# Performance work log

Measured on AMD Instinct MI355X. Metric: run time of the kernel, lower is better.

## Reference

```python
import jax, jax.numpy as jnp
import numpy as np

B, S, D, H = 4, 2048, 1024, 16
HD = D // H

def setup_inputs() -> dict:
    key = jax.random.key(0)
    ks = jax.random.split(key, 6)
    scale = 0.02
    return {
        "x": jax.random.normal(ks[0], (B, S, D), jnp.float32),
        "Wq": jax.random.normal(ks[1], (D, D), jnp.float32) * scale,
        "Wk": jax.random.normal(ks[2], (D, D), jnp.float32) * scale,
        "Wv": jax.random.normal(ks[3], (D, D), jnp.float32) * scale,
        "Wo": jax.random.normal(ks[4], (D, D), jnp.float32) * scale,
        "bo": jnp.zeros((D,), jnp.float32),
    }

def reference(x, Wq, Wk, Wv, Wo, bo):
    b, s, _ = x.shape
    # separate Q/K/V projections (no bias, qkv_bias=False)
    q = jnp.einsum('bsd,ed->bse', x, Wq).reshape(b, s, H, HD).transpose(0, 2, 1, 3)
    k = jnp.einsum('bsd,ed->bse', x, Wk).reshape(b, s, H, HD).transpose(0, 2, 1, 3)
    v = jnp.einsum('bsd,ed->bse', x, Wv).reshape(b, s, H, HD).transpose(0, 2, 1, 3)
    # full [B,H,S,S] scores, causal mask, scaled softmax (matches torch order:
    # mask applied to raw scores, then divide by sqrt(head_dim))
    scores = jnp.einsum('bhqd,bhkd->bhqk', q, k)
    causal = jnp.tril(jnp.ones((s, s), bool))
    scores = jnp.where(causal, scores, -jnp.inf)
    attn = jax.nn.softmax(scores / np.float32(np.sqrt(HD)), axis=-1)
    # dropout=0.0 -> identity in eval
    ctx = jnp.einsum('bhqk,bhkd->bhqd', attn, v)
    ctx = ctx.transpose(0, 2, 1, 3).reshape(b, s, D)
    return jnp.einsum('bsd,ed->bse', ctx, Wo) + bo
```

## Files before the change

### kernel.cpp

```cpp
#include <hip/hip_runtime.h>
#include <stdint.h>

#define DEVI __device__ __forceinline__

typedef __attribute__((ext_vector_type(8))) short bf16x8;
typedef __attribute__((ext_vector_type(8))) unsigned short u16x8;
typedef __attribute__((ext_vector_type(4))) float f32x4;
typedef unsigned short u16;
typedef unsigned int u32;

constexpr int B = 4, S = 2048, D = 1024, H = 16;
constexpr int BS = B * S;
constexpr int QS = 3 * D;
constexpr float CS = 0.18033688011112042f;

DEVI u16 f2bf(float f) {
  u32 u = __float_as_uint(f);
  u32 r = (u + 0x7FFFu + ((u >> 16) & 1u)) >> 16;
  return (u16)r;
}

DEVI void async_load16(const void* g, void* l) {
  __builtin_amdgcn_global_load_lds((const __attribute__((address_space(1))) u32*)g,
                                   (__attribute__((address_space(3))) u32*)l, 16, 0, 0);
}

__global__ void cast_f32_bf16(const float* __restrict__ in, u16* __restrict__ out, int n4) {
  int i = blockIdx.x * blockDim.x + threadIdx.x;
  if (i >= n4) return;
  float4 v = ((const float4*)in)[i];
  ushort4 o;
  o.x = f2bf(v.x); o.y = f2bf(v.y); o.z = f2bf(v.z); o.w = f2bf(v.w);
  ((ushort4*)out)[i] = o;
}

__global__ void cast_w4(const float* __restrict__ wq, const float* __restrict__ wk,
                        const float* __restrict__ wv, const float* __restrict__ wo,
                        u16* __restrict__ wqkv, u16* __restrict__ wob, int n4) {
  int i = blockIdx.x * blockDim.x + threadIdx.x;
  if (i >= n4) return;
  int y = blockIdx.y;
  const float* src = (y == 0) ? wq : (y == 1) ? wk : (y == 2) ? wv : wo;
  u16* dst = (y < 3) ? (wqkv + (size_t)y * D * D) : wob;
  float4 v = ((const float4*)src)[i];
  ushort4 o;
  o.x = f2bf(v.x); o.y = f2bf(v.y); o.z = f2bf(v.z); o.w = f2bf(v.w);
  ((ushort4*)dst)[i] = o;
}

template<int STORE_BF16, int ADD_BIAS, int SCALE_QCOLS>
__global__ __launch_bounds__(256)
void gemm_bt(const u16* __restrict__ A, const u16* __restrict__ Bt,
             const float* __restrict__ bias, void* __restrict__ Cout,
             int M, int N, int K) {
  __shared__ u16 a_lds[2][128 * 32];
  __shared__ u16 b_lds[2][128 * 32];
  const int tid = threadIdx.x, lane = tid & 63, wv = tid >> 6;
  const int m0 = blockIdx.x * 128, n0 = blockIdx.y * 128;
  const int wm = (wv >> 1) * 64, wn = (wv & 1) * 64;
  const int fr = lane & 15, fk = (lane >> 4) * 8;

  f32x4 acc[4][4] = {};

  const int seg = wv * 2;
  const int srow = seg * 16 + (lane >> 2);
  const int scolb = (lane & 3) * 16;
  const char* ab = (const char*)A + ((size_t)(m0 + srow) * K) * 2 + scolb;
  const char* bb = (const char*)Bt + ((size_t)(n0 + srow) * K) * 2 + scolb;
  const size_t row16 = (size_t)16 * K * 2;

  {
    char* adst = (char*)a_lds[0] + seg * 1024;
    char* bdst = (char*)b_lds[0] + seg * 1024;
    async_load16(ab, adst);
    async_load16(ab + row16, adst + 1024);
    async_load16(bb, bdst);
    async_load16(bb + row16, bdst + 1024);
    ab += 64; bb += 64;
  }
  int cur = 0;

  for (int k0 = 0; k0 < K; k0 += 32) {
    asm volatile("s_waitcnt vmcnt(0)" ::: "memory");
    asm volatile("s_barrier" ::: "memory");
    bf16x8 af[4], bfr[4];
    #pragma unroll
    for (int i = 0; i < 4; ++i) {
      af[i]  = *(const bf16x8*)&a_lds[cur][(wm + i * 16 + fr) * 32 + fk];
      bfr[i] = *(const bf16x8*)&b_lds[cur][(wn + i * 16 + fr) * 32 + fk];
    }
    if (k0 + 32 < K) {
      char* adst = (char*)a_lds[cur ^ 1] + seg * 1024;
      char* bdst = (char*)b_lds[cur ^ 1] + seg * 1024;
      async_load16(ab, adst);
      async_load16(ab + row16, adst + 1024);
      async_load16(bb, bdst);
      async_load16(bb + row16, bdst + 1024);
      ab += 64; bb += 64;
    }
    #pragma unroll
    for (int i = 0; i < 4; ++i)
      #pragma unroll
      for (int j = 0; j < 4; ++j)
        acc[i][j] = __builtin_amdgcn_mfma_f32_16x16x32_bf16(af[i], bfr[j], acc[i][j], 0, 0, 0);
    cur ^= 1;
  }

  const int cr = (lane >> 4) * 4, cc = lane & 15;
  const float qsc = (SCALE_QCOLS && n0 < 1024) ? CS : 1.0f;
  #pragma unroll
  for (int j = 0; j < 4; ++j) {
    int gn = n0 + wn + j * 16 + cc;
    float bv = ADD_BIAS ? bias[gn] : 0.0f;
    #pragma unroll
    for (int i = 0; i < 4; ++i) {
      #pragma unroll
      for (int r = 0; r < 4; ++r) {
        size_t idx = (size_t)(m0 + wm + i * 16 + cr + r) * N + gn;
        float v = acc[i][j][r];
        if (SCALE_QCOLS) v *= qsc;
        v += bv;
        if (STORE_BF16) ((u16*)Cout)[idx] = f2bf(v);
        else            ((float*)Cout)[idx] = v;
      }
    }
  }
}

__global__ __launch_bounds__(256, 2)
void attn_kernel(const u16* __restrict__ Q, const u16* __restrict__ K,
                 const u16* __restrict__ V, u16* __restrict__ C) {
  __shared__ u16 vt_lds[2][64 * 72];
  __shared__ u16 p_lds[4][32 * 72];

  const int tid = threadIdx.x, lane = tid & 63, wv = tid >> 6;
  const int f = blockIdx.x;
  const int pair = (f >> 3) & 7;
  const int g = (f & 7) | ((f >> 6) << 3);
  const int h = g & 15, b = g >> 4;

  const int fr = lane & 15, hi = lane >> 4, fk = hi * 8;
  const int cr = hi * 4, cc = fr;

  const size_t base = (size_t)(b * S) * QS + h * 64;
  const size_t cbase = (size_t)(b * S) * D + h * 64;

  const int vd0 = (tid & 7) * 8;
  const int vkvp = tid >> 3;
  const u16* Vg = V + base;
  const u16* Kg = K + base;

  for (int half = 0; half < 2; ++half) {
    const int qt = half ? (15 - pair) : pair;
    const int q0 = qt * 128;
    const int qw = q0 + wv * 32;

    bf16x8 qf[2][2];
    {
      const u16* Qp = Q + base + (size_t)qw * QS;
      #pragma unroll
      for (int mi = 0; mi < 2; ++mi)
        #pragma unroll
        for (int kc = 0; kc < 2; ++kc)
          qf[mi][kc] = *(const bf16x8*)(Qp + (size_t)(mi * 16 + fr) * QS + kc * 32 + fk);
    }

    f32x4 ctx[2][4] = {};
    float lr[2][4] = {};

    const int nt = q0 / 64 + 2;

    u16x8 v0a, v0b, v1a, v1b;
    {
      const u16* vr = Vg + (size_t)(vkvp * 2) * QS + vd0;
      v0a = *(const u16x8*)vr;
      v0b = *(const u16x8*)(vr + QS);
    }
    int cur = 0;

    for (int t = 0; t < nt; ++t) {
      const int kv0 = t * 64;
      const bool part = (kv0 <= qw + 31);
      const bool more = (t + 1 < nt);

      {
        #pragma unroll
        for (int i = 0; i < 8; ++i) {
          int d = vd0 + i;
          int kvp = vkvp ^ (((d >> 3) & 7) << 2);
          u32 w = (u32)(u16)v0a[i] | ((u32)(u16)v0b[i] << 16);
          *(u32*)&vt_lds[cur][d * 72 + kvp * 2] = w;
        }
      }

      bf16x8 kf[4][2];
      if (part) {
        const u16* kp = Kg + (size_t)(kv0 + fr) * QS + fk;
        #pragma unroll
        for (int ni = 0; ni < 4; ++ni)
          #pragma unroll
          for (int kc = 0; kc < 2; ++kc)
            kf[ni][kc] = *(const bf16x8*)(kp + (size_t)(ni * 16) * QS + kc * 32);
      }
      if (more) {
        const u16* vr = Vg + (size_t)((t + 1) * 64 + vkvp * 2) * QS + vd0;
        v1a = *(const u16x8*)vr;
        v1b = *(const u16x8*)(vr + QS);
      }

      asm volatile("s_waitcnt lgkmcnt(0)" ::: "memory");
      asm volatile("s_barrier" ::: "memory");

      if (part) {
        f32x4 sc[2][4] = {};
        __builtin_amdgcn_s_setprio(1);
        #pragma unroll
        for (int mi = 0; mi < 2; ++mi)
          #pragma unroll
          for (int ni = 0; ni < 4; ++ni)
            #pragma unroll
            for (int kc = 0; kc < 2; ++kc)
              sc[mi][ni] = __builtin_amdgcn_mfma_f32_16x16x32_bf16(qf[mi][kc], kf[ni][kc], sc[mi][ni], 0, 0, 0);
        __builtin_amdgcn_s_setprio(0);

        if (kv0 + 63 > qw) {
          #pragma unroll
          for (int mi = 0; mi < 2; ++mi)
            #pragma unroll
            for (int ni = 0; ni < 4; ++ni)
              #pragma unroll
              for (int r = 0; r < 4; ++r) {
                int qrow = qw + mi * 16 + cr + r;
                int kvc = kv0 + ni * 16 + cc;
                if (kvc > qrow) sc[mi][ni][r] = -3.0e38f;
              }
        }

        #pragma unroll
        for (int mi = 0; mi < 2; ++mi)
          #pragma unroll
          for (int ni = 0; ni < 4; ++ni)
            #pragma unroll
            for (int r = 0; r < 4; ++r)
              sc[mi][ni][r] = exp2f(sc[mi][ni][r]);
        #pragma unroll
        for (int mi = 0; mi < 2; ++mi)
          #pragma unroll
          for (int r = 0; r < 4; ++r) {
            float rs = (sc[mi][0][r] + sc[mi][1][r]) + (sc[mi][2][r] + sc[mi][3][r]);
            rs += __shfl_xor(rs, 1);
            rs += __shfl_xor(rs, 2);
            rs += __shfl_xor(rs, 4);
            rs += __shfl_xor(rs, 8);
            lr[mi][r] += rs;
          }

        #pragma unroll
        for (int mi = 0; mi < 2; ++mi)
          #pragma unroll
          for (int ni = 0; ni < 4; ++ni)
            #pragma unroll
            for (int r = 0; r < 4; ++r)
              p_lds[wv][(mi * 16 + cr + r) * 72 + ni * 16 + cc] = f2bf(sc[mi][ni][r]);

        asm volatile("s_waitcnt lgkmcnt(0)" ::: "memory");
        __builtin_amdgcn_sched_barrier(0);

        bf16x8 pa[2][2], vf[4][2];
        #pragma unroll
        for (int mi = 0; mi < 2; ++mi)
          #pragma unroll
          for (int kc = 0; kc < 2; ++kc)
            pa[mi][kc] = *(const bf16x8*)&p_lds[wv][(mi * 16 + fr) * 72 + kc * 32 + fk];
        #pragma unroll
        for (int db = 0; db < 4; ++db)
          #pragma unroll
          for (int kc = 0; kc < 2; ++kc) {
            int d = db * 16 + fr;
            int kvp = (kc * 16 + hi * 4) ^ (((d >> 3) & 7) << 2);
            vf[db][kc] = *(const bf16x8*)&vt_lds[cur][d * 72 + kvp * 2];
          }
        __builtin_amdgcn_s_setprio(1);
        #pragma unroll
        for (int mi = 0; mi < 2; ++mi)
          #pragma unroll
          for (int db = 0; db < 4; ++db)
            #pragma unroll
            for (int kc = 0; kc < 2; ++kc)
              ctx[mi][db] = __builtin_amdgcn_mfma_f32_16x16x32_bf16(pa[mi][kc], vf[db][kc], ctx[mi][db], 0, 0, 0);
        __builtin_amdgcn_s_setprio(0);
      }

      if (more) { v0a = v1a; v0b = v1b; }
      cur ^= 1;
    }

    u16* Cp = C + cbase + (size_t)qw * D;
    #pragma unroll
    for (int mi = 0; mi < 2; ++mi)
      #pragma unroll
      for (int r = 0; r < 4; ++r) {
        float inv = 1.0f / lr[mi][r];
        #pragma unroll
        for (int db = 0; db < 4; ++db)
          Cp[(size_t)(mi * 16 + cr + r) * D + db * 16 + cc] = f2bf(ctx[mi][db][r] * inv);
      }
  }
}

extern "C" void kernel_launch(void* const* d_in, const int* in_sizes, int n_in,
                              void* d_out, int out_size, void* d_ws, size_t ws_size,
                              hipStream_t stream) {
  const float* x  = (const float*)d_in[0];
  const float* Wq = (const float*)d_in[1];
  const float* Wk = (const float*)d_in[2];
  const float* Wv = (const float*)d_in[3];
  const float* Wo = (const float*)d_in[4];
  const float* bo = (const float*)d_in[5];

  char* ws = (char*)d_ws;
  u16* xb    = (u16*)(ws + 0);
  u16* Wqkvb = (u16*)(ws + (16u << 20));
  u16* Wob   = (u16*)(ws + (22u << 20));
  u16* QKVb  = (u16*)(ws + (24u << 20));
  u16* Cb    = (u16*)(ws + (72u << 20));

  const int XN = BS * D;
  const int WN = D * D;

  cast_f32_bf16<<<XN / 4 / 256, 256, 0, stream>>>(x, xb, XN / 4);
  cast_w4<<<dim3(WN / 4 / 256, 4), 256, 0, stream>>>(Wq, Wk, Wv, Wo, Wqkvb, Wob, WN / 4);

  gemm_bt<1, 0, 1><<<dim3(BS / 128, QS / 128), dim3(256), 0, stream>>>(xb, Wqkvb, nullptr, QKVb, BS, QS, D);

  attn_kernel<<<dim3(512), dim3(256), 0, stream>>>(QKVb, QKVb + D, QKVb + 2 * D, Cb);

  gemm_bt<0, 1, 0><<<dim3(BS / 128, D / 128), dim3(256), 0, stream>>>(Cb, Wob, bo, d_out, BS, D, D);
}
```

Before: 288.0 us.

## Shrink attention query tiles to 64 rows and triple-buffer GEMM LDS

The attention kernel now processes 64-row query tiles, with 16 rows per wave instead of 32. This doubles the grid to 1024 blocks and raises launch bounds to 4 blocks per CU, giving more parallelism and finer causal load balance at the cost of less K/V reuse per block. The GEMM moves from double- to triple-buffered LDS staging with a partial vmcnt wait, keeping two tiles of async loads in flight to hide global latency. This uses more LDS per block, which may reduce GEMM occupancy.

```diff
diff --git a/kernel.cpp b/kernel.cpp
--- a/kernel.cpp
+++ b/kernel.cpp
@@ -53,8 +53,8 @@
 void gemm_bt(const u16* __restrict__ A, const u16* __restrict__ Bt,
              const float* __restrict__ bias, void* __restrict__ Cout,
              int M, int N, int K) {
-  __shared__ u16 a_lds[2][128 * 32];
-  __shared__ u16 b_lds[2][128 * 32];
+  __shared__ u16 a_lds[3][128 * 32];
+  __shared__ u16 b_lds[3][128 * 32];
   const int tid = threadIdx.x, lane = tid & 63, wv = tid >> 6;
   const int m0 = blockIdx.x * 128, n0 = blockIdx.y * 128;
   const int wm = (wv >> 1) * 64, wn = (wv & 1) * 64;
@@ -69,19 +69,25 @@
   const char* bb = (const char*)Bt + ((size_t)(n0 + srow) * K) * 2 + scolb;
   const size_t row16 = (size_t)16 * K * 2;
 
-  {
-    char* adst = (char*)a_lds[0] + seg * 1024;
-    char* bdst = (char*)b_lds[0] + seg * 1024;
+  const int nsteps = K / 32;
+
+  auto stage = [&](int bufid) {
+    char* adst = (char*)a_lds[bufid] + seg * 1024;
+    char* bdst = (char*)b_lds[bufid] + seg * 1024;
     async_load16(ab, adst);
     async_load16(ab + row16, adst + 1024);
     async_load16(bb, bdst);
     async_load16(bb + row16, bdst + 1024);
     ab += 64; bb += 64;
-  }
+  };
+
+  stage(0);
+  if (nsteps > 1) stage(1);
+
   int cur = 0;
-
-  for (int k0 = 0; k0 < K; k0 += 32) {
-    asm volatile("s_waitcnt vmcnt(0)" ::: "memory");
+  for (int t = 0; t < nsteps; ++t) {
+    if (t < nsteps - 1) asm volatile("s_waitcnt vmcnt(4)" ::: "memory");
+    else                asm volatile("s_waitcnt vmcnt(0)" ::: "memory");
     asm volatile("s_barrier" ::: "memory");
     bf16x8 af[4], bfr[4];
     #pragma unroll
@@ -89,21 +95,16 @@
       af[i]  = *(const bf16x8*)&a_lds[cur][(wm + i * 16 + fr) * 32 + fk];
       bfr[i] = *(const bf16x8*)&b_lds[cur][(wn + i * 16 + fr) * 32 + fk];
     }
-    if (k0 + 32 < K) {
-      char* adst = (char*)a_lds[cur ^ 1] + seg * 1024;
-      char* bdst = (char*)b_lds[cur ^ 1] + seg * 1024;
-      async_load16(ab, adst);
-      async_load16(ab + row16, adst + 1024);
-      async_load16(bb, bdst);
-      async_load16(bb + row16, bdst + 1024);
-      ab += 64; bb += 64;
+    if (t + 2 < nsteps) {
+      int nxt = cur + 2; if (nxt >= 3) nxt -= 3;
+      stage(nxt);
     }
     #pragma unroll
     for (int i = 0; i < 4; ++i)
       #pragma unroll
       for (int j = 0; j < 4; ++j)
         acc[i][j] = __builtin_amdgcn_mfma_f32_16x16x32_bf16(af[i], bfr[j], acc[i][j], 0, 0, 0);
-    cur ^= 1;
+    cur = (cur == 2) ? 0 : cur + 1;
   }
 
   const int cr = (lane >> 4) * 4, cc = lane & 15;
@@ -127,16 +128,16 @@
   }
 }
 
-__global__ __launch_bounds__(256, 2)
+__global__ __launch_bounds__(256, 4)
 void attn_kernel(const u16* __restrict__ Q, const u16* __restrict__ K,
                  const u16* __restrict__ V, u16* __restrict__ C) {
   __shared__ u16 vt_lds[2][64 * 72];
-  __shared__ u16 p_lds[4][32 * 72];
+  __shared__ u16 p_lds[4][16 * 72];
 
   const int tid = threadIdx.x, lane = tid & 63, wv = tid >> 6;
   const int f = blockIdx.x;
-  const int pair = (f >> 3) & 7;
-  const int g = (f & 7) | ((f >> 6) << 3);
+  const int pr = (f >> 3) & 15;
+  const int g = (f & 7) | ((f >> 7) << 3);
   const int h = g & 15, b = g >> 4;
 
   const int fr = lane & 15, hi = lane >> 4, fk = hi * 8;
@@ -150,25 +151,25 @@
   const u16* Vg = V + base;
   const u16* Kg = K + base;
 
+  int cur = 0;
+
   for (int half = 0; half < 2; ++half) {
-    const int qt = half ? (15 - pair) : pair;
-    const int q0 = qt * 128;
-    const int qw = q0 + wv * 32;
-
-    bf16x8 qf[2][2];
+    const int qt = half ? (31 - pr) : pr;
+    const int q0 = qt * 64;
+    const int qw = q0 + wv * 16;
+
+    bf16x8 qf[2];
     {
-      const u16* Qp = Q + base + (size_t)qw * QS;
-      #pragma unroll
-      for (int mi = 0; mi < 2; ++mi)
-        #pragma unroll
-        for (int kc = 0; kc < 2; ++kc)
-          qf[mi][kc] = *(const bf16x8*)(Qp + (size_t)(mi * 16 + fr) * QS + kc * 32 + fk);
-    }
-
-    f32x4 ctx[2][4] = {};
-    float lr[2][4] = {};
-
-    const int nt = q0 / 64 + 2;
+      const u16* Qp = Q + base + (size_t)(qw + fr) * QS;
+      #pragma unroll
+      for (int kc = 0; kc < 2; ++kc)
+        qf[kc] = *(const bf16x8*)(Qp + kc * 32 + fk);
+    }
+
+    f32x4 ctx[4] = {};
+    float lr[4] = {};
+
+    const int nt = qt + 1;
 
     u16x8 v0a, v0b, v1a, v1b;
     {
@@ -176,11 +177,9 @@
       v0a = *(const u16x8*)vr;
       v0b = *(const u16x8*)(vr + QS);
     }
-    int cur = 0;
 
     for (int t = 0; t < nt; ++t) {
       const int kv0 = t * 64;
-      const bool part = (kv0 <= qw + 31);
       const bool more = (t + 1 < nt);
 
       {
@@ -194,7 +193,7 @@
       }
 
       bf16x8 kf[4][2];
-      if (part) {
+      {
         const u16* kp = Kg + (size_t)(kv0 + fr) * QS + fk;
         #pragma unroll
         for (int ni = 0; ni < 4; ++ni)
@@ -211,85 +210,69 @@
       asm volatile("s_waitcnt lgkmcnt(0)" ::: "memory");
       asm volatile("s_barrier" ::: "memory");
 
-      if (part) {
-        f32x4 sc[2][4] = {};
-        __builtin_amdgcn_s_setprio(1);
-        #pragma unroll
-        for (int mi = 0; mi < 2; ++mi)
-          #pragma unroll
-          for (int ni = 0; ni < 4; ++ni)
-            #pragma unroll
-            for (int kc = 0; kc < 2; ++kc)
-              sc[mi][ni] = __builtin_amdgcn_mfma_f32_16x16x32_bf16(qf[mi][kc], kf[ni][kc], sc[mi][ni], 0, 0, 0);
-        __builtin_amdgcn_s_setprio(0);
-
-        if (kv0 + 63 > qw) {
-          #pragma unroll
-          for (int mi = 0; mi < 2; ++mi)
-            #pragma unroll
-            for (int ni = 0; ni < 4; ++ni)
-              #pragma unroll
-              for (int r = 0; r < 4; ++r) {
-                int qrow = qw + mi * 16 + cr + r;
-                int kvc = kv0 + ni * 16 + cc;
-                if (kvc > qrow) sc[mi][ni][r] = -3.0e38f;
-              }
-        }
-
-        #pragma unroll
-        for (int mi = 0; mi < 2; ++mi)
-          #pragma unroll
-          for (int ni = 0; ni < 4; ++ni)
-            #pragma unroll
-            for (int r = 0; r < 4; ++r)
-              sc[mi][ni][r] = exp2f(sc[mi][ni][r]);
-        #pragma unroll
-        for (int mi = 0; mi < 2; ++mi)
+      f32x4 sc[4] = {};
+      __builtin_amdgcn_s_setprio(1);
+      #pragma unroll
+      for (int ni = 0; ni < 4; ++ni)
+        #pragma unroll
+        for (int kc = 0; kc < 2; ++kc)
+          sc[ni] = __builtin_amdgcn_mfma_f32_16x16x32_bf16(qf[kc], kf[ni][kc], sc[ni], 0, 0, 0);
+      __builtin_amdgcn_s_setprio(0);
+
+      if (t == nt - 1) {
+        #pragma unroll
+        for (int ni = 0; ni < 4; ++ni)
           #pragma unroll
           for (int r = 0; r < 4; ++r) {
-            float rs = (sc[mi][0][r] + sc[mi][1][r]) + (sc[mi][2][r] + sc[mi][3][r]);
-            rs += __shfl_xor(rs, 1);
-            rs += __shfl_xor(rs, 2);
-            rs += __shfl_xor(rs, 4);
-            rs += __shfl_xor(rs, 8);
-            lr[mi][r] += rs;
+            int qrow = qw + cr + r;
+            int kvc = kv0 + ni * 16 + cc;
+            if (kvc > qrow) sc[ni][r] = -3.0e38f;
           }
-
-        #pragma unroll
-        for (int mi = 0; mi < 2; ++mi)
-          #pragma unroll
-          for (int ni = 0; ni < 4; ++ni)
-            #pragma unroll
-            for (int r = 0; r < 4; ++r)
-              p_lds[wv][(mi * 16 + cr + r) * 72 + ni * 16 + cc] = f2bf(sc[mi][ni][r]);
-
-        asm volatile("s_waitcnt lgkmcnt(0)" ::: "memory");
-        __builtin_amdgcn_sched_barrier(0);
-
-        bf16x8 pa[2][2], vf[4][2];
-        #pragma unroll
-        for (int mi = 0; mi < 2; ++mi)
-          #pragma unroll
-          for (int kc = 0; kc < 2; ++kc)
-            pa[mi][kc] = *(const bf16x8*)&p_lds[wv][(mi * 16 + fr) * 72 + kc * 32 + fk];
-        #pragma unroll
-        for (int db = 0; db < 4; ++db)
-          #pragma unroll
-          for (int kc = 0; kc < 2; ++kc) {
-            int d = db * 16 + fr;
-            int kvp = (kc * 16 + hi * 4) ^ (((d >> 3) & 7) << 2);
-            vf[db][kc] = *(const bf16x8*)&vt_lds[cur][d * 72 + kvp * 2];
-          }
-        __builtin_amdgcn_s_setprio(1);
-        #pragma unroll
-        for (int mi = 0; mi < 2; ++mi)
-          #pragma unroll
-          for (int db = 0; db < 4; ++db)
-            #pragma unroll
-            for (int kc = 0; kc < 2; ++kc)
-              ctx[mi][db] = __builtin_amdgcn_mfma_f32_16x16x32_bf16(pa[mi][kc], vf[db][kc], ctx[mi][db], 0, 0, 0);
-        __builtin_amdgcn_s_setprio(0);
-      }
+      }
+
+      #pragma unroll
+      for (int ni = 0; ni < 4; ++ni)
+        #pragma unroll
+        for (int r = 0; r < 4; ++r)
+          sc[ni][r] = exp2f(sc[ni][r]);
+      #pragma unroll
+      for (int r = 0; r < 4; ++r) {
+        float rs = (sc[0][r] + sc[1][r]) + (sc[2][r] + sc[3][r]);
+        rs += __shfl_xor(rs, 1);
+        rs += __shfl_xor(rs, 2);
+        rs += __shfl_xor(rs, 4);
+        rs += __shfl_xor(rs, 8);
+        lr[r] += rs;
+      }
+
+      #pragma unroll
+      for (int ni = 0; ni < 4; ++ni)
+        #pragma unroll
+        for (int r = 0; r < 4; ++r)
+          p_lds[wv][(cr + r) * 72 + ni * 16 + cc] = f2bf(sc[ni][r]);
+
+      asm volatile("s_waitcnt lgkmcnt(0)" ::: "memory");
+      __builtin_amdgcn_sched_barrier(0);
+
+      bf16x8 pa[2], vf[4][2];
+      #pragma unroll
+      for (int kc = 0; kc < 2; ++kc)
+        pa[kc] = *(const bf16x8*)&p_lds[wv][fr * 72 + kc * 32 + fk];
+      #pragma unroll
+      for (int db = 0; db < 4; ++db)
+        #pragma unroll
+        for (int kc = 0; kc < 2; ++kc) {
+          int d = db * 16 + fr;
+          int kvp = (kc * 16 + hi * 4) ^ (((d >> 3) & 7) << 2);
+          vf[db][kc] = *(const bf16x8*)&vt_lds[cur][d * 72 + kvp * 2];
+        }
+      __builtin_amdgcn_s_setprio(1);
+      #pragma unroll
+      for (int db = 0; db < 4; ++db)
+        #pragma unroll
+        for (int kc = 0; kc < 2; ++kc)
+          ctx[db] = __builtin_amdgcn_mfma_f32_16x16x32_bf16(pa[kc], vf[db][kc], ctx[db], 0, 0, 0);
+      __builtin_amdgcn_s_setprio(0);
 
       if (more) { v0a = v1a; v0b = v1b; }
       cur ^= 1;
@@ -297,14 +280,12 @@
 
     u16* Cp = C + cbase + (size_t)qw * D;
     #pragma unroll
-    for (int mi = 0; mi < 2; ++mi)
-      #pragma unroll
-      for (int r = 0; r < 4; ++r) {
-        float inv = 1.0f / lr[mi][r];
-        #pragma unroll
-        for (int db = 0; db < 4; ++db)
-          Cp[(size_t)(mi * 16 + cr + r) * D + db * 16 + cc] = f2bf(ctx[mi][db][r] * inv);
-      }
+    for (int r = 0; r < 4; ++r) {
+      float inv = 1.0f / lr[r];
+      #pragma unroll
+      for (int db = 0; db < 4; ++db)
+        Cp[(size_t)(cr + r) * D + db * 16 + cc] = f2bf(ctx[db][r] * inv);
+    }
   }
 }
 
@@ -333,7 +314,7 @@
 
   gemm_bt<1, 0, 1><<<dim3(BS / 128, QS / 128), dim3(256), 0, stream>>>(xb, Wqkvb, nullptr, QKVb, BS, QS, D);
 
-  attn_kernel<<<dim3(512), dim3(256), 0, stream>>>(QKVb, QKVb + D, QKVb + 2 * D, Cb);
+  attn_kernel<<<dim3(1024), dim3(256), 0, stream>>>(QKVb, QKVb + D, QKVb + 2 * D, Cb);
 
   gemm_bt<0, 1, 0><<<dim3(BS / 128, D / 128), dim3(256), 0, stream>>>(Cb, Wob, bo, d_out, BS, D, D);
 }
```

After: 323.2 us. 1.12x slower.
